# Kernel tuning notes

Hardware: AMD Instinct MI355X
Metric: run time of the kernel (lower is better)

The kernel has to match this reference:

```python
import jax, jax.numpy as jnp
import numpy as np

B, T, D_MODEL, D_HEAD = 8, 2048, 1024, 64


def setup_inputs() -> dict:
    key = jax.random.key(0)
    kx, kq, kk, kv = jax.random.split(key, 4)
    scale = 1.0 / np.sqrt(D_MODEL)
    return {
        "x": jax.random.normal(kx, (B, T, D_MODEL), dtype=jnp.float32),
        "Wq": jax.random.normal(kq, (D_MODEL, D_HEAD), dtype=jnp.float32) * scale,
        "Wk": jax.random.normal(kk, (D_MODEL, D_HEAD), dtype=jnp.float32) * scale,
        "Wv": jax.random.normal(kv, (D_MODEL, D_HEAD), dtype=jnp.float32) * scale,
    }


def reference(x, Wq, Wk, Wv):
    # x: [B, T, C]; single-head causal self-attention (naive, full T x T scores).
    Bn, Tn, C = x.shape
    q = x @ Wq  # [B, T, d_head]
    k = x @ Wk
    v = x @ Wv
    # NOTE: original scales by sqrt(C) = sqrt(d_model), not sqrt(d_head).
    wei = jnp.einsum("btd,bsd->bts", q, k) / jnp.sqrt(jnp.asarray(C, x.dtype))
    causal = jnp.tril(jnp.ones((Tn, Tn), dtype=bool))  # tril[:T,:T]
    wei = jnp.where(causal, wei, -jnp.inf)
    wei = jax.nn.softmax(wei, axis=-1)
    # dropout p=0.0 (deterministic / eval mode) -> identity
    out = jnp.einsum("bts,bsd->btd", wei, v)  # [B, T, d_head]
    return out
```

## Files before the change

kernel.cpp:

```cpp
#include <hip/hip_runtime.h>
#include <hip/hip_bf16.h>

#define DM 1024
#define DH 64
#define TT 2048

typedef __attribute__((ext_vector_type(8))) short bf16x8;
typedef __attribute__((ext_vector_type(4))) short s16x4;
typedef __attribute__((ext_vector_type(4))) float f32x4;

static __device__ __forceinline__ short f2bf(float f) {
  union { __hip_bfloat16 h; short s; } u;
  u.h = __float2bfloat16(f);
  return u.s;
}

__global__ __launch_bounds__(256) void convw_kernel(const float* __restrict__ Wq,
                                                    const float* __restrict__ Wk,
                                                    const float* __restrict__ Wv,
                                                    short* __restrict__ Wt) {
  int idx = blockIdx.x * 256 + threadIdx.x;
  if (idx >= 3 * 64 * 1024) return;
  int wsel = idx >> 16;
  int rem  = idx & 65535;
  int n = rem >> 10;
  int k = rem & 1023;
  const float* W = (wsel == 0) ? Wq : (wsel == 1) ? Wk : Wv;
  Wt[idx] = f2bf(W[k * DH + n]);
}

__global__ __launch_bounds__(512, 4) void proj_kernel(const float* __restrict__ x,
                                                      const short* __restrict__ Wt,
                                                      short* __restrict__ Qb,
                                                      short* __restrict__ Kb,
                                                      short* __restrict__ Vt) {
  __shared__ short As[64 * 64];
  __shared__ short Bs[192 * 64];
  char* Ab = (char*)As;
  char* Bb = (char*)Bs;
  int tid  = threadIdx.x;
  int lane = tid & 63;
  int wid  = tid >> 6;
  int l15 = lane & 15, lq = lane >> 4;
  int wr = wid >> 1, wc = wid & 1;
  int row0 = blockIdx.x * 64;

  int arow = tid >> 3, acg = tid & 7;
  const float* axp = x + (size_t)(row0 + arow) * DM + acg * 8;
  int abyte = arow * 128 + ((acg * 16) ^ ((arow & 7) << 4));
  int brow = tid >> 1, bh = tid & 1;
  const short* bwp = Wt + (size_t)brow * DM + bh * 32;
  int bswz = (brow & 7) << 4;
  int bbyte[4];
  #pragma unroll
  for (int i = 0; i < 4; ++i) bbyte[i] = brow * 128 + ((bh * 64 + i * 16) ^ bswz);

  float4 pa0 = ((const float4*)axp)[0];
  float4 pa1 = ((const float4*)axp)[1];
  bf16x8 pb[4];
  if (tid < 384) {
    #pragma unroll
    for (int i = 0; i < 4; ++i) pb[i] = ((const bf16x8*)bwp)[i];
  }

  f32x4 acc[6];
  #pragma unroll
  for (int n = 0; n < 6; ++n) acc[n] = (f32x4){0.f, 0.f, 0.f, 0.f};

  for (int s = 0; s < 16; ++s) {
    bf16x8 aw;
    aw[0] = f2bf(pa0.x); aw[1] = f2bf(pa0.y); aw[2] = f2bf(pa0.z); aw[3] = f2bf(pa0.w);
    aw[4] = f2bf(pa1.x); aw[5] = f2bf(pa1.y); aw[6] = f2bf(pa1.z); aw[7] = f2bf(pa1.w);
    *(bf16x8*)(Ab + abyte) = aw;
    if (tid < 384) {
      #pragma unroll
      for (int i = 0; i < 4; ++i) *(bf16x8*)(Bb + bbyte[i]) = pb[i];
    }
    __syncthreads();
    if (s < 15) {
      const float* nax = axp + (s + 1) * 64;
      pa0 = ((const float4*)nax)[0];
      pa1 = ((const float4*)nax)[1];
      if (tid < 384) {
        const short* nbw = bwp + (s + 1) * 64;
        #pragma unroll
        for (int i = 0; i < 4; ++i) pb[i] = ((const bf16x8*)nbw)[i];
      }
    }
    #pragma unroll
    for (int kk = 0; kk < 2; ++kk) {
      int koff = (kk * 64 + lq * 16) ^ ((l15 & 7) << 4);
      bf16x8 af = *(const bf16x8*)(Ab + (wr * 16 + l15) * 128 + koff);
      bf16x8 bf[6];
      #pragma unroll
      for (int nc = 0; nc < 6; ++nc)
        bf[nc] = *(const bf16x8*)(Bb + (wc * 96 + nc * 16 + l15) * 128 + koff);
      #pragma unroll
      for (int nc = 0; nc < 6; ++nc)
        acc[nc] = __builtin_amdgcn_mfma_f32_16x16x32_bf16(af, bf[nc], acc[nc], 0, 0, 0);
    }
    __syncthreads();
  }

  int growb = row0 + wr * 16 + lq * 4;
  #pragma unroll
  for (int nc = 0; nc < 6; ++nc) {
    int gcolb = wc * 96 + nc * 16;
    int mat = gcolb >> 6;
    int mc  = (gcolb & 63) + l15;
    if (mat == 0) {
      #pragma unroll
      for (int r = 0; r < 4; ++r)
        Qb[(size_t)(growb + r) * DH + mc] = f2bf(acc[nc][r]);
    } else if (mat == 1) {
      #pragma unroll
      for (int r = 0; r < 4; ++r)
        Kb[(size_t)(growb + r) * DH + mc] = f2bf(acc[nc][r]);
    } else {
      int b = growb >> 11;
      int tl = growb & 2047;
      s16x4 pk;
      #pragma unroll
      for (int r = 0; r < 4; ++r) pk[r] = f2bf(acc[nc][r]);
      *(s16x4*)(Vt + ((size_t)(b * DH + mc)) * TT + tl) = pk;
    }
  }
}

__global__ __launch_bounds__(512) void flash_kernel(const short* __restrict__ Qb,
                                                    const short* __restrict__ Kb,
                                                    const short* __restrict__ Vt,
                                                    float* __restrict__ out) {
  __shared__ union ShBuf {
    short Pl[8][16][72];
    float Om[8][16][64];
  } sh;
  __shared__ float Mm[8][16];
  __shared__ float Lm[8][16];
  __shared__ float Sc[8][16];
  __shared__ float Linv[16];
  int w    = threadIdx.x >> 6;
  int lane = threadIdx.x & 63;
  int l15 = lane & 15, lq = lane >> 4;
  int qt = 127 - (blockIdx.x >> 3);
  int b  = blockIdx.x & 7;
  int row0 = qt * 16;

  const short* qp = Qb + ((size_t)(b * TT + row0 + l15)) * DH + 8 * lq;
  bf16x8 qf0 = *reinterpret_cast<const bf16x8*>(qp);
  bf16x8 qf1 = *reinterpret_cast<const bf16x8*>(qp + 32);

  float mrow[4] = {-1e30f, -1e30f, -1e30f, -1e30f};
  float lrow[4] = {0.f, 0.f, 0.f, 0.f};
  f32x4 o[4];
  #pragma unroll
  for (int nt = 0; nt < 4; ++nt) o[nt] = (f32x4){0.f, 0.f, 0.f, 0.f};

  int nkt = (qt >> 2) + 1;
  for (int kt = w; kt < nkt; kt += 8) {
    int k0 = kt * 64;
    f32x4 s[4];
    #pragma unroll
    for (int nt = 0; nt < 4; ++nt) s[nt] = (f32x4){0.f, 0.f, 0.f, 0.f};
    #pragma unroll
    for (int nt = 0; nt < 4; ++nt) {
      const short* kp = Kb + ((size_t)(b * TT + k0 + nt * 16 + l15)) * DH + 8 * lq;
      bf16x8 b0 = *reinterpret_cast<const bf16x8*>(kp);
      bf16x8 b1 = *reinterpret_cast<const bf16x8*>(kp + 32);
      s[nt] = __builtin_amdgcn_mfma_f32_16x16x32_bf16(qf0, b0, s[nt], 0, 0, 0);
      s[nt] = __builtin_amdgcn_mfma_f32_16x16x32_bf16(qf1, b1, s[nt], 0, 0, 0);
    }
    float rmax[4] = {-1e30f, -1e30f, -1e30f, -1e30f};
    #pragma unroll
    for (int nt = 0; nt < 4; ++nt) {
      int key = k0 + nt * 16 + l15;
      #pragma unroll
      for (int r = 0; r < 4; ++r) {
        int qr = row0 + lq * 4 + r;
        float v = s[nt][r] * 0.03125f;
        v = (key <= qr) ? v : -1e30f;
        s[nt][r] = v;
        rmax[r] = fmaxf(rmax[r], v);
      }
    }
    #pragma unroll
    for (int r = 0; r < 4; ++r)
      #pragma unroll
      for (int d = 1; d < 16; d <<= 1)
        rmax[r] = fmaxf(rmax[r], __shfl_xor(rmax[r], d));
    float alpha[4], rs[4];
    #pragma unroll
    for (int r = 0; r < 4; ++r) {
      float mn = fmaxf(mrow[r], rmax[r]);
      alpha[r] = __expf(mrow[r] - mn);
      mrow[r] = mn;
      rs[r] = 0.f;
    }
    #pragma unroll
    for (int nt = 0; nt < 4; ++nt)
      #pragma unroll
      for (int r = 0; r < 4; ++r) {
        float p = __expf(s[nt][r] - mrow[r]);
        s[nt][r] = p;
        rs[r] += p;
      }
    #pragma unroll
    for (int r = 0; r < 4; ++r) {
      #pragma unroll
      for (int d = 1; d < 16; d <<= 1)
        rs[r] += __shfl_xor(rs[r], d);
      lrow[r] = lrow[r] * alpha[r] + rs[r];
    }
    #pragma unroll
    for (int nt = 0; nt < 4; ++nt) {
      o[nt][0] *= alpha[0]; o[nt][1] *= alpha[1];
      o[nt][2] *= alpha[2]; o[nt][3] *= alpha[3];
    }
    #pragma unroll
    for (int nt = 0; nt < 4; ++nt)
      #pragma unroll
      for (int r = 0; r < 4; ++r)
        sh.Pl[w][lq * 4 + r][nt * 16 + l15] = f2bf(s[nt][r]);
    bf16x8 pa0 = *reinterpret_cast<const bf16x8*>(&sh.Pl[w][l15][8 * lq]);
    bf16x8 pa1 = *reinterpret_cast<const bf16x8*>(&sh.Pl[w][l15][32 + 8 * lq]);
    #pragma unroll
    for (int nt = 0; nt < 4; ++nt) {
      const short* vp = Vt + ((size_t)(b * DH + nt * 16 + l15)) * TT + k0 + 8 * lq;
      bf16x8 v0 = *reinterpret_cast<const bf16x8*>(vp);
      bf16x8 v1 = *reinterpret_cast<const bf16x8*>(vp + 32);
      o[nt] = __builtin_amdgcn_mfma_f32_16x16x32_bf16(pa0, v0, o[nt], 0, 0, 0);
      o[nt] = __builtin_amdgcn_mfma_f32_16x16x32_bf16(pa1, v1, o[nt], 0, 0, 0);
    }
  }
  __syncthreads();
  #pragma unroll
  for (int nt = 0; nt < 4; ++nt)
    #pragma unroll
    for (int r = 0; r < 4; ++r)
      sh.Om[w][lq * 4 + r][nt * 16 + l15] = o[nt][r];
  if (l15 == 0) {
    #pragma unroll
    for (int r = 0; r < 4; ++r) {
      Mm[w][lq * 4 + r] = mrow[r];
      Lm[w][lq * 4 + r] = lrow[r];
    }
  }
  __syncthreads();
  if (threadIdx.x < 16) {
    int row = threadIdx.x;
    float M = -1e30f;
    #pragma unroll
    for (int v = 0; v < 8; ++v) M = fmaxf(M, Mm[v][row]);
    float L = 0.f;
    #pragma unroll
    for (int v = 0; v < 8; ++v) {
      float sv = __expf(Mm[v][row] - M);
      Sc[v][row] = sv;
      L += Lm[v][row] * sv;
    }
    Linv[row] = 1.0f / L;
  }
  __syncthreads();
  int e = threadIdx.x;
  #pragma unroll
  for (int i = 0; i < 2; ++i, e += 512) {
    int row = e >> 6, col = e & 63;
    float val = 0.f;
    #pragma unroll
    for (int v = 0; v < 8; ++v) val += sh.Om[v][row][col] * Sc[v][row];
    out[((size_t)(b * TT + row0 + row)) * DH + col] = val * Linv[row];
  }
}

extern "C" void kernel_launch(void* const* d_in, const int* in_sizes, int n_in,
                              void* d_out, int out_size, void* d_ws, size_t ws_size,
                              hipStream_t stream) {
  const float* x  = (const float*)d_in[0];
  const float* Wq = (const float*)d_in[1];
  const float* Wk = (const float*)d_in[2];
  const float* Wv = (const float*)d_in[3];
  float* out = (float*)d_out;
  char* ws = (char*)d_ws;
  short* Qb = (short*)(ws);
  short* Kb = (short*)(ws + (2ull << 20));
  short* Vt = (short*)(ws + (4ull << 20));
  short* Wt = (short*)(ws + (6ull << 20));

  convw_kernel<<<dim3(768), dim3(256), 0, stream>>>(Wq, Wk, Wv, Wt);
  proj_kernel<<<dim3(256), dim3(512), 0, stream>>>(x, Wt, Qb, Kb, Vt);
  flash_kernel<<<dim3(1024), dim3(512), 0, stream>>>(Qb, Kb, Vt, out);
}
```

Baseline: 153.9 us.

## Use 128-key tiles with 4 waves per block and fold scale into Q

The flash kernel now runs 4 waves per block instead of 8, and each wave handles 128-key tiles (pairs of 64-key tiles), so softmax reductions and rescaling are amortised over twice as many keys. The 1/32 score scale moves into the Q projection epilogue, which removes a multiply per score. The cost is more registers per wave and fewer waves splitting each query tile's key range, which makes per-block latency worse on short causal rows. Reading up to 64 keys past the causal diagonal is handled by the mask, and those keys stay in bounds for the top query tiles.

```diff
diff --git a/kernel.cpp b/kernel.cpp
--- a/kernel.cpp
+++ b/kernel.cpp
@@ -111,7 +111,7 @@
     if (mat == 0) {
       #pragma unroll
       for (int r = 0; r < 4; ++r)
-        Qb[(size_t)(growb + r) * DH + mc] = f2bf(acc[nc][r]);
+        Qb[(size_t)(growb + r) * DH + mc] = f2bf(acc[nc][r] * 0.03125f);
     } else if (mat == 1) {
       #pragma unroll
       for (int r = 0; r < 4; ++r)
@@ -127,17 +127,17 @@
   }
 }
 
-__global__ __launch_bounds__(512) void flash_kernel(const short* __restrict__ Qb,
-                                                    const short* __restrict__ Kb,
-                                                    const short* __restrict__ Vt,
-                                                    float* __restrict__ out) {
+__global__ __launch_bounds__(256, 4) void flash_kernel(const short* __restrict__ Qb,
+                                                       const short* __restrict__ Kb,
+                                                       const short* __restrict__ Vt,
+                                                       float* __restrict__ out) {
   __shared__ union ShBuf {
-    short Pl[8][16][72];
-    float Om[8][16][64];
+    short Pl[4][16][136];
+    float Om[4][16][64];
   } sh;
-  __shared__ float Mm[8][16];
-  __shared__ float Lm[8][16];
-  __shared__ float Sc[8][16];
+  __shared__ float Mm[4][16];
+  __shared__ float Lm[4][16];
+  __shared__ float Sc[4][16];
   __shared__ float Linv[16];
   int w    = threadIdx.x >> 6;
   int lane = threadIdx.x & 63;
@@ -157,27 +157,28 @@
   for (int nt = 0; nt < 4; ++nt) o[nt] = (f32x4){0.f, 0.f, 0.f, 0.f};
 
   int nkt = (qt >> 2) + 1;
-  for (int kt = w; kt < nkt; kt += 8) {
-    int k0 = kt * 64;
-    f32x4 s[4];
-    #pragma unroll
-    for (int nt = 0; nt < 4; ++nt) s[nt] = (f32x4){0.f, 0.f, 0.f, 0.f};
-    #pragma unroll
-    for (int nt = 0; nt < 4; ++nt) {
+  int npair = (nkt + 1) >> 1;
+  for (int p = w; p < npair; p += 4) {
+    int k0 = p * 128;
+    f32x4 s[8];
+    #pragma unroll
+    for (int nt = 0; nt < 8; ++nt) {
       const short* kp = Kb + ((size_t)(b * TT + k0 + nt * 16 + l15)) * DH + 8 * lq;
       bf16x8 b0 = *reinterpret_cast<const bf16x8*>(kp);
       bf16x8 b1 = *reinterpret_cast<const bf16x8*>(kp + 32);
-      s[nt] = __builtin_amdgcn_mfma_f32_16x16x32_bf16(qf0, b0, s[nt], 0, 0, 0);
-      s[nt] = __builtin_amdgcn_mfma_f32_16x16x32_bf16(qf1, b1, s[nt], 0, 0, 0);
+      f32x4 t = (f32x4){0.f, 0.f, 0.f, 0.f};
+      t = __builtin_amdgcn_mfma_f32_16x16x32_bf16(qf0, b0, t, 0, 0, 0);
+      t = __builtin_amdgcn_mfma_f32_16x16x32_bf16(qf1, b1, t, 0, 0, 0);
+      s[nt] = t;
     }
     float rmax[4] = {-1e30f, -1e30f, -1e30f, -1e30f};
     #pragma unroll
-    for (int nt = 0; nt < 4; ++nt) {
+    for (int nt = 0; nt < 8; ++nt) {
       int key = k0 + nt * 16 + l15;
       #pragma unroll
       for (int r = 0; r < 4; ++r) {
         int qr = row0 + lq * 4 + r;
-        float v = s[nt][r] * 0.03125f;
+        float v = s[nt][r];
         v = (key <= qr) ? v : -1e30f;
         s[nt][r] = v;
         rmax[r] = fmaxf(rmax[r], v);
@@ -197,12 +198,12 @@
       rs[r] = 0.f;
     }
     #pragma unroll
-    for (int nt = 0; nt < 4; ++nt)
+    for (int nt = 0; nt < 8; ++nt)
       #pragma unroll
       for (int r = 0; r < 4; ++r) {
-        float p = __expf(s[nt][r] - mrow[r]);
-        s[nt][r] = p;
-        rs[r] += p;
+        float pv = __expf(s[nt][r] - mrow[r]);
+        s[nt][r] = pv;
+        rs[r] += pv;
       }
     #pragma unroll
     for (int r = 0; r < 4; ++r) {
@@ -217,19 +218,22 @@
       o[nt][2] *= alpha[2]; o[nt][3] *= alpha[3];
     }
     #pragma unroll
-    for (int nt = 0; nt < 4; ++nt)
+    for (int nt = 0; nt < 8; ++nt)
       #pragma unroll
       for (int r = 0; r < 4; ++r)
         sh.Pl[w][lq * 4 + r][nt * 16 + l15] = f2bf(s[nt][r]);
-    bf16x8 pa0 = *reinterpret_cast<const bf16x8*>(&sh.Pl[w][l15][8 * lq]);
-    bf16x8 pa1 = *reinterpret_cast<const bf16x8*>(&sh.Pl[w][l15][32 + 8 * lq]);
+    bf16x8 pa[4];
+    #pragma unroll
+    for (int h = 0; h < 4; ++h)
+      pa[h] = *reinterpret_cast<const bf16x8*>(&sh.Pl[w][l15][h * 32 + 8 * lq]);
     #pragma unroll
     for (int nt = 0; nt < 4; ++nt) {
       const short* vp = Vt + ((size_t)(b * DH + nt * 16 + l15)) * TT + k0 + 8 * lq;
-      bf16x8 v0 = *reinterpret_cast<const bf16x8*>(vp);
-      bf16x8 v1 = *reinterpret_cast<const bf16x8*>(vp + 32);
-      o[nt] = __builtin_amdgcn_mfma_f32_16x16x32_bf16(pa0, v0, o[nt], 0, 0, 0);
-      o[nt] = __builtin_amdgcn_mfma_f32_16x16x32_bf16(pa1, v1, o[nt], 0, 0, 0);
+      #pragma unroll
+      for (int h = 0; h < 4; ++h) {
+        bf16x8 vf = *reinterpret_cast<const bf16x8*>(vp + 32 * h);
+        o[nt] = __builtin_amdgcn_mfma_f32_16x16x32_bf16(pa[h], vf, o[nt], 0, 0, 0);
+      }
     }
   }
   __syncthreads();
@@ -250,10 +254,10 @@
     int row = threadIdx.x;
     float M = -1e30f;
     #pragma unroll
-    for (int v = 0; v < 8; ++v) M = fmaxf(M, Mm[v][row]);
+    for (int v = 0; v < 4; ++v) M = fmaxf(M, Mm[v][row]);
     float L = 0.f;
     #pragma unroll
-    for (int v = 0; v < 8; ++v) {
+    for (int v = 0; v < 4; ++v) {
       float sv = __expf(Mm[v][row] - M);
       Sc[v][row] = sv;
       L += Lm[v][row] * sv;
@@ -263,11 +267,11 @@
   __syncthreads();
   int e = threadIdx.x;
   #pragma unroll
-  for (int i = 0; i < 2; ++i, e += 512) {
+  for (int i = 0; i < 4; ++i, e += 256) {
     int row = e >> 6, col = e & 63;
     float val = 0.f;
     #pragma unroll
-    for (int v = 0; v < 8; ++v) val += sh.Om[v][row][col] * Sc[v][row];
+    for (int v = 0; v < 4; ++v) val += sh.Om[v][row][col] * Sc[v][row];
     out[((size_t)(b * TT + row0 + row)) * DH + col] = val * Linv[row];
   }
 }
@@ -288,5 +292,5 @@
 
   convw_kernel<<<dim3(768), dim3(256), 0, stream>>>(Wq, Wk, Wv, Wt);
   proj_kernel<<<dim3(256), dim3(512), 0, stream>>>(x, Wt, Qb, Kb, Vt);
-  flash_kernel<<<dim3(1024), dim3(512), 0, stream>>>(Qb, Kb, Vt, out);
-}
+  flash_kernel<<<dim3(1024), dim3(256), 0, stream>>>(Qb, Kb, Vt, out);
+}
```

After: 154.9 us. Within noise of the previous version (+0.7%).
